# Kernel tuning notes

Hardware: AMD Instinct MI355X
Metric: run time of the kernel (lower is better)

Reference implementation:

```python
import jax, jax.numpy as jnp
import numpy as np

B, S, HID = 2, 2048, 2048
NH, NKV, HD = 16, 4, 128
ROT = 64            # head_dim * partial_rotary_factor
WINDOW = 512        # sliding_window_size
ROPE_BASE = 10000.0


def setup_inputs() -> dict:
    key = jax.random.key(0)
    ks = jax.random.split(key, 5)
    scale = 0.02
    return {
        "hidden_states": jax.random.normal(ks[0], (B, S, HID), jnp.float32),
        "Wq": jax.random.normal(ks[1], (NH * HD, HID), jnp.float32) * scale,
        "Wk": jax.random.normal(ks[2], (NKV * HD, HID), jnp.float32) * scale,
        "Wv": jax.random.normal(ks[3], (NKV * HD, HID), jnp.float32) * scale,
        "Wo": jax.random.normal(ks[4], (HID, NH * HD), jnp.float32) * scale,
    }


def _rope_cos_sin(seq_len, dtype):
    inv_freq = 1.0 / (ROPE_BASE ** (jnp.arange(0, ROT, 2, dtype=jnp.float32) / ROT))
    t = jnp.arange(seq_len, dtype=jnp.float32)
    freqs = t[:, None] * inv_freq[None, :]          # [S, ROT/2]
    emb = jnp.concatenate([freqs, freqs], axis=-1)   # [S, ROT]
    return jnp.cos(emb).astype(dtype), jnp.sin(emb).astype(dtype)


def _rotate_half(x):
    x1, x2 = x[..., : x.shape[-1] // 2], x[..., x.shape[-1] // 2:]
    return jnp.concatenate([-x2, x1], axis=-1)


def reference(hidden_states, Wq, Wk, Wv, Wo):
    b, s, _ = hidden_states.shape
    n_rep = NH // NKV

    q = (hidden_states @ Wq.T).reshape(b, s, NH, HD).transpose(0, 2, 1, 3)    # [B,NH,S,HD]
    k = (hidden_states @ Wk.T).reshape(b, s, NKV, HD).transpose(0, 2, 1, 3)   # [B,NKV,S,HD]
    v = (hidden_states @ Wv.T).reshape(b, s, NKV, HD).transpose(0, 2, 1, 3)

    # partial rotary embedding on the first ROT dims
    cos, sin = _rope_cos_sin(s, q.dtype)   # [S, ROT]
    cos = cos[None, None]                  # broadcast over batch, heads
    sin = sin[None, None]
    q_rot, q_pass = q[..., :ROT], q[..., ROT:]
    k_rot, k_pass = k[..., :ROT], k[..., ROT:]
    q_rot = q_rot * cos + _rotate_half(q_rot) * sin
    k_rot = k_rot * cos + _rotate_half(k_rot) * sin
    q = jnp.concatenate([q_rot, q_pass], axis=-1)
    k = jnp.concatenate([k_rot, k_pass], axis=-1)

    # GQA: repeat kv heads
    k = jnp.repeat(k, n_rep, axis=1)   # [B,NH,S,HD]
    v = jnp.repeat(v, n_rep, axis=1)

    scores = jnp.einsum("bhqd,bhkd->bhqk", q, k) / jnp.sqrt(jnp.asarray(HD, q.dtype))

    # sliding-window causal mask: allow j in [i-WINDOW+1, i]
    i = jnp.arange(s)[:, None]
    j = jnp.arange(s)[None, :]
    allowed = (j <= i) & (j > i - WINDOW)
    scores = jnp.where(allowed[None, None], scores, -jnp.inf)

    attn = jax.nn.softmax(scores.astype(jnp.float32), axis=-1).astype(q.dtype)
    out = jnp.einsum("bhqk,bhkd->bhqd", attn, v)          # [B,NH,S,HD]
    out = out.transpose(0, 2, 1, 3).reshape(b, s, NH * HD)
    return out @ Wo.T
```

## Files before the change

kernel.cpp:

```cpp
#include <hip/hip_runtime.h>
#include <cstdint>
#include <cstddef>

typedef __bf16 bf16;
typedef __attribute__((ext_vector_type(8))) __bf16 bf16x8;
typedef __attribute__((ext_vector_type(4))) __bf16 bf16x4;
typedef __attribute__((ext_vector_type(4))) float f32x4;
typedef __attribute__((ext_vector_type(4))) short s16x4;

#define S_LEN   2048
#define WIN     512
#define NH_Q    16
#define NH_KV   4
#define HD_     128
#define NTOK    4096

#if defined(__has_builtin)
#if __has_builtin(__builtin_amdgcn_mfma_f32_16x16x16bf16_1k)
#define HAVE_MFMA16 1
#endif
#endif
#ifndef HAVE_MFMA16
#define HAVE_MFMA16 0
#endif

#define WAIT_VM4   0x0F74
#define WAIT_VM2   0x0F72
#define WAIT_VM0   0x0F70
#define CFENCE() __asm__ __volatile__("" ::: "memory")

__device__ __forceinline__ void async_copy16(const void* g, void* l) {
  __builtin_amdgcn_global_load_lds(
      (const __attribute__((address_space(1))) void*)g,
      (__attribute__((address_space(3))) void*)l, 16, 0, 0);
}

__global__ __launch_bounds__(256)
void cvt_all(const float* __restrict__ hs, const float* __restrict__ wq,
             const float* __restrict__ wk, const float* __restrict__ wv,
             const float* __restrict__ wo, bf16* __restrict__ hsb,
             bf16* __restrict__ wqb, bf16* __restrict__ wkb,
             bf16* __restrict__ wvb, bf16* __restrict__ wob) {
  long i = ((long)blockIdx.x * 256 + threadIdx.x) * 4;
  const float* in;
  bf16* out;
  if (i < 8388608)       { in = hs + i;            out = hsb + i; }
  else if (i < 12582912) { in = wq + (i - 8388608); out = wqb + (i - 8388608); }
  else if (i < 13631488) { in = wk + (i - 12582912); out = wkb + (i - 12582912); }
  else if (i < 14680064) { in = wv + (i - 13631488); out = wvb + (i - 13631488); }
  else                   { in = wo + (i - 14680064); out = wob + (i - 14680064); }
  float4 v = *(const float4*)in;
  bf16x4 t = {(bf16)v.x, (bf16)v.y, (bf16)v.z, (bf16)v.w};
  *(bf16x4*)out = t;
}

template <typename OutT>
__global__ __launch_bounds__(256)
void gemm_bt(const bf16* __restrict__ A, const bf16* __restrict__ W,
             OutT* __restrict__ C, int M, int N, int K) {
  __shared__ __align__(16) bf16 As[2][128 * 32];
  __shared__ __align__(16) bf16 Bs[2][128 * 32];
  const int tid  = threadIdx.x;
  const int wave = tid >> 6, lane = tid & 63;
  const int quad = lane >> 4, l16 = lane & 15;
  const int wm = wave >> 1, wn = wave & 1;
  const int m0 = blockIdx.y * 128, n0 = blockIdx.x * 128;
  const int lrow = lane >> 2;
  const int lcol = (((lane & 3) + ((lane >> 3) & 3)) & 3) * 8;
  const int gfrag = ((quad - ((l16 >> 1) & 3)) & 3) * 8;

  f32x4 acc[4][4];
#pragma unroll
  for (int i = 0; i < 4; ++i)
#pragma unroll
    for (int j = 0; j < 4; ++j) acc[i][j] = (f32x4){0.f, 0.f, 0.f, 0.f};

  auto stage = [&](int buf, int k0) {
#pragma unroll
    for (int it = 0; it < 2; ++it) {
      const int c   = it * 4 + wave;
      const int row = c * 16 + lrow;
      async_copy16(A + (size_t)(m0 + row) * K + k0 + lcol, &As[buf][c * 512]);
      async_copy16(W + (size_t)(n0 + row) * K + k0 + lcol, &Bs[buf][c * 512]);
    }
  };

  stage(0, 0);
  __syncthreads();
  for (int k0 = 0; k0 < K; k0 += 32) {
    const int cur = (k0 >> 5) & 1;
    if (k0 + 32 < K) stage(cur ^ 1, k0 + 32);
    bf16x8 af[4], bfr[4];
#pragma unroll
    for (int mt = 0; mt < 4; ++mt)
      af[mt] = *(const bf16x8*)&As[cur][(wm * 64 + mt * 16 + l16) * 32 + gfrag];
#pragma unroll
    for (int nt = 0; nt < 4; ++nt)
      bfr[nt] = *(const bf16x8*)&Bs[cur][(wn * 64 + nt * 16 + l16) * 32 + gfrag];
#pragma unroll
    for (int mt = 0; mt < 4; ++mt)
#pragma unroll
      for (int nt = 0; nt < 4; ++nt)
        acc[mt][nt] = __builtin_amdgcn_mfma_f32_16x16x32_bf16(
            af[mt], bfr[nt], acc[mt][nt], 0, 0, 0);
    __syncthreads();
  }
#pragma unroll
  for (int mt = 0; mt < 4; ++mt)
#pragma unroll
    for (int nt = 0; nt < 4; ++nt)
#pragma unroll
      for (int r = 0; r < 4; ++r) {
        const int row = m0 + wm * 64 + mt * 16 + quad * 4 + r;
        const int col = n0 + wn * 64 + nt * 16 + l16;
        C[(size_t)row * N + col] = (OutT)acc[mt][nt][r];
      }
}

__global__ __launch_bounds__(512, 2)
void gemm_qkv8(const bf16* __restrict__ A, const bf16* __restrict__ Wq,
               const bf16* __restrict__ Wk, const bf16* __restrict__ Wv,
               bf16* __restrict__ Qo, bf16* __restrict__ Ko,
               bf16* __restrict__ Vt) {
  __shared__ __align__(16) char smem[131072];
  const int tid  = threadIdx.x;
  const int wave = tid >> 6, lane = tid & 63;
  const int quad = lane >> 4, l16 = lane & 15;
  const int wm = wave >> 2, wn = wave & 3;

  const int flat = blockIdx.y * 12 + blockIdx.x;
  const int swz  = (flat & 7) * 24 + (flat >> 3);
  const int m0 = (swz / 12) * 256;
  const int n0 = (swz % 12) * 256;

  const int rdb = (l16 * 64 + quad * 16) ^ ((l16 & 8) << 2);

  const int srow = lane >> 2;
  const int scol = ((lane & 3) * 8) ^ ((lane >> 5) << 4);
  const bf16* asrc = A + (size_t)(m0 + srow) * 2048 + scol;
  const bf16* aptr[2][2];
  int adst[2][2];
#pragma unroll
  for (int mh = 0; mh < 2; ++mh)
#pragma unroll
    for (int j = 0; j < 2; ++j) {
      const int rb = j * 8 + mh * 4 + (wave >> 1);
      aptr[mh][j] = asrc + (size_t)rb * 16 * 2048 + (wave & 1) * 32;
      adst[mh][j] = (rb * 2 + (wave & 1)) << 10;
    }
  const bf16* bptr[2][2];
  int bdst[2][2];
#pragma unroll
  for (int nh = 0; nh < 2; ++nh)
#pragma unroll
    for (int j = 0; j < 2; ++j) {
      const int rb = j * 8 + (wave >> 2) * 4 + nh * 2 + ((wave >> 1) & 1);
      const int nrow = n0 + rb * 16 + srow;
      const bf16* p = nrow < 2048 ? Wq + (size_t)nrow * 2048
                    : nrow < 2560 ? Wk + (size_t)(nrow - 2048) * 2048
                                  : Wv + (size_t)(nrow - 2560) * 2048;
      bptr[nh][j] = p + scol + (wave & 1) * 32;
      bdst[nh][j] = (rb * 2 + (wave & 1)) << 10;
    }

#define STAGE_A(mh, tt) do {                                        \
    char* _b = smem + ((tt) & 1) * 32768;                           \
    async_copy16(aptr[mh][0] + (tt) * 64, _b + adst[mh][0]);        \
    async_copy16(aptr[mh][1] + (tt) * 64, _b + adst[mh][1]);        \
  } while (0)
#define STAGE_B(nh, tt) do {                                        \
    char* _b = smem + 65536 + ((tt) & 1) * 32768;                   \
    async_copy16(bptr[nh][0] + (tt) * 64, _b + bdst[nh][0]);        \
    async_copy16(bptr[nh][1] + (tt) * 64, _b + bdst[nh][1]);        \
  } while (0)

  f32x4 acc[8][4];
#pragma unroll
  for (int i = 0; i < 8; ++i)
#pragma unroll
    for (int j = 0; j < 4; ++j) acc[i][j] = (f32x4){0.f, 0.f, 0.f, 0.f};

  bf16x8 afr[4][2];
  bf16x8 bfr[2][2][2];

  auto read_a = [&](const char* Ab, int mh) __attribute__((always_inline)) {
#pragma unroll
    for (int mt = 0; mt < 4; ++mt)
#pragma unroll
      for (int ks = 0; ks < 2; ++ks)
        afr[mt][ks] = *(const bf16x8*)(
            Ab + (((wm * 8 + mh * 4 + mt) * 2 + ks) << 10) + rdb);
  };
  auto read_b = [&](const char* Bb, int nh) __attribute__((always_inline)) {
#pragma unroll
    for (int nt = 0; nt < 2; ++nt)
#pragma unroll
      for (int ks = 0; ks < 2; ++ks)
        bfr[nh][nt][ks] = *(const bf16x8*)(
            Bb + (((wn * 4 + nh * 2 + nt) * 2 + ks) << 10) + rdb);
  };
  auto do_mfma = [&](int mh, int nh) __attribute__((always_inline)) {
    __builtin_amdgcn_s_setprio(1);
#pragma unroll
    for (int mt = 0; mt < 4; ++mt)
#pragma unroll
      for (int nt = 0; nt < 2; ++nt)
#pragma unroll
        for (int ks = 0; ks < 2; ++ks)
          acc[mh * 4 + mt][nh * 2 + nt] = __builtin_amdgcn_mfma_f32_16x16x32_bf16(
              afr[mt][ks], bfr[nh][nt][ks], acc[mh * 4 + mt][nh * 2 + nt],
              0, 0, 0);
    __builtin_amdgcn_s_setprio(0);
  };

  STAGE_A(0, 0); STAGE_B(0, 0); STAGE_B(1, 0); STAGE_A(1, 0);
  CFENCE();

  for (int t = 0; t < 31; ++t) {
    const char* Ab = smem + (t & 1) * 32768;
    const char* Bb = smem + 65536 + (t & 1) * 32768;
    const int nx = t + 1;
    __builtin_amdgcn_s_waitcnt(WAIT_VM4); CFENCE();
    __builtin_amdgcn_s_barrier(); CFENCE();
    read_a(Ab, 0); read_b(Bb, 0);
    STAGE_A(0, nx); CFENCE();
    do_mfma(0, 0);
    __builtin_amdgcn_s_waitcnt(WAIT_VM4); CFENCE();
    __builtin_amdgcn_s_barrier(); CFENCE();
    read_b(Bb, 1);
    STAGE_B(0, nx); CFENCE();
    do_mfma(0, 1);
    __builtin_amdgcn_s_waitcnt(WAIT_VM4); CFENCE();
    __builtin_amdgcn_s_barrier(); CFENCE();
    read_a(Ab, 1);
    STAGE_B(1, nx); CFENCE();
    do_mfma(1, 0);
    __builtin_amdgcn_s_barrier(); CFENCE();
    STAGE_A(1, nx); CFENCE();
    do_mfma(1, 1);
  }
  {
    const char* Ab = smem + 32768;
    const char* Bb = smem + 65536 + 32768;
    __builtin_amdgcn_s_waitcnt(WAIT_VM4); CFENCE();
    __builtin_amdgcn_s_barrier(); CFENCE();
    read_a(Ab, 0); read_b(Bb, 0);
    do_mfma(0, 0);
    __builtin_amdgcn_s_waitcnt(WAIT_VM2); CFENCE();
    __builtin_amdgcn_s_barrier(); CFENCE();
    read_b(Bb, 1);
    do_mfma(0, 1);
    __builtin_amdgcn_s_waitcnt(WAIT_VM0); CFENCE();
    __builtin_amdgcn_s_barrier(); CFENCE();
    read_a(Ab, 1);
    do_mfma(1, 0);
    do_mfma(1, 1);
  }
#undef STAGE_A
#undef STAGE_B

  const int cbase = n0 + wn * 64;
  if (cbase < 2560 && (cbase & 127) == 0) {
#pragma unroll
    for (int nt = 0; nt < 2; ++nt) {
      const int d = nt * 16 + l16;
      const float invf = exp2f(-(float)d * 0.41524101186091903f);
#pragma unroll
      for (int mt = 0; mt < 8; ++mt)
#pragma unroll
        for (int r = 0; r < 4; ++r) {
          const int pos = (m0 + wm * 128 + mt * 16 + quad * 4 + r) & (S_LEN - 1);
          float s, c;
          __sincosf((float)pos * invf, &s, &c);
          const float x1 = acc[mt][nt][r], x2 = acc[mt][nt + 2][r];
          acc[mt][nt][r]     = x1 * c - x2 * s;
          acc[mt][nt + 2][r] = x2 * c + x1 * s;
        }
    }
  }
#pragma unroll
  for (int mt = 0; mt < 8; ++mt) {
    const int row0 = m0 + wm * 128 + mt * 16 + quad * 4;
#pragma unroll
    for (int nt = 0; nt < 4; ++nt) {
      const int col16 = cbase + nt * 16;
      if (col16 < 2048) {
#pragma unroll
        for (int r = 0; r < 4; ++r)
          Qo[(size_t)(row0 + r) * 2048 + col16 + l16] = (bf16)acc[mt][nt][r];
      } else if (col16 < 2560) {
#pragma unroll
        for (int r = 0; r < 4; ++r)
          Ko[(size_t)(row0 + r) * 512 + col16 - 2048 + l16] = (bf16)acc[mt][nt][r];
      } else {
        const int colv = col16 + l16 - 2560;
        const int b = row0 >> 11, s0 = row0 & (S_LEN - 1);
        bf16x4 tq = {(bf16)acc[mt][nt][0], (bf16)acc[mt][nt][1],
                     (bf16)acc[mt][nt][2], (bf16)acc[mt][nt][3]};
        *(bf16x4*)(Vt + ((size_t)(b * NH_KV + (colv >> 7)) * HD_ + (colv & 127))
                        * S_LEN + s0) = tq;
      }
    }
  }
}

#define KS_STRIDE 136
#define VT_STRIDE 72

__global__ __launch_bounds__(256)
void attn_kernel(const bf16* __restrict__ Qg, const bf16* __restrict__ Kg,
                 const bf16* __restrict__ Vtg, bf16* __restrict__ Og) {
  __shared__ __align__(16) bf16 Ks[64 * KS_STRIDE];
  __shared__ __align__(16) bf16 Vt[128 * VT_STRIDE];
#if !HAVE_MFMA16
  __shared__ __align__(16) bf16 Pb[4][16 * 72];
#endif
  const int tid  = threadIdx.x;
  const int wave = tid >> 6, lane = tid & 63;
  const int quad = lane >> 4, l16 = lane & 15;
  const int qt = blockIdx.x, h = blockIdx.y, b = blockIdx.z;
  const int kv = h >> 2;
  const int q0 = qt * 64;
  const int tok0 = b * S_LEN;
  const float scale = 0.08838834764831845f;
  const int q = q0 + wave * 16 + l16;

  bf16x8 qf[4];
  {
    const bf16* qp = Qg + (size_t)(tok0 + q) * (NH_Q * HD_) + h * HD_ + quad * 8;
#pragma unroll
    for (int kb = 0; kb < 4; ++kb) qf[kb] = *(const bf16x8*)(qp + kb * 32);
  }

  f32x4 o[8];
#pragma unroll
  for (int dt = 0; dt < 8; ++dt) o[dt] = (f32x4){0.f, 0.f, 0.f, 0.f};
  float m_run = -__builtin_inff(), l_run = 0.f;

  int kt_begin = q0 - WIN;
  if (kt_begin < 0) kt_begin = 0;
  const int kt_end = q0 + 64;
  const bf16* vt_base = Vtg + (size_t)(b * NH_KV + kv) * HD_ * S_LEN;

  for (int kt = kt_begin; kt < kt_end; kt += 64) {
    __syncthreads();
#pragma unroll
    for (int it = 0; it < 4; ++it) {
      int vid = tid + it * 256;
      int key = vid >> 4, dblk = vid & 15;
      bf16x8 v = *(const bf16x8*)(Kg + (size_t)(tok0 + kt + key) * (NH_KV * HD_)
                                  + kv * HD_ + dblk * 8);
      *(bf16x8*)&Ks[key * KS_STRIDE + dblk * 8] = v;
    }
#pragma unroll
    for (int it = 0; it < 4; ++it) {
      int vid = tid + it * 256;
      int d = vid >> 3, kblk = vid & 7;
      bf16x8 v = *(const bf16x8*)(vt_base + (size_t)d * S_LEN + kt + kblk * 8);
      *(bf16x8*)&Vt[d * VT_STRIDE + kblk * 8] = v;
    }
    __syncthreads();

    f32x4 st[4];
#pragma unroll
    for (int nt = 0; nt < 4; ++nt) {
      f32x4 acc = (f32x4){0.f, 0.f, 0.f, 0.f};
#pragma unroll
      for (int kb = 0; kb < 4; ++kb) {
        bf16x8 kf = *(const bf16x8*)&Ks[(nt * 16 + l16) * KS_STRIDE + kb * 32 + quad * 8];
        acc = __builtin_amdgcn_mfma_f32_16x16x32_bf16(kf, qf[kb], acc, 0, 0, 0);
      }
      st[nt] = acc;
    }
#pragma unroll
    for (int nt = 0; nt < 4; ++nt)
#pragma unroll
      for (int r = 0; r < 4; ++r) {
        int key = kt + nt * 16 + quad * 4 + r;
        bool ok = (key <= q) && (key > q - WIN);
        st[nt][r] = ok ? st[nt][r] * scale : -__builtin_inff();
      }
    float mx = -__builtin_inff();
#pragma unroll
    for (int nt = 0; nt < 4; ++nt)
#pragma unroll
      for (int r = 0; r < 4; ++r) mx = fmaxf(mx, st[nt][r]);
    mx = fmaxf(mx, __shfl_xor(mx, 16, 64));
    mx = fmaxf(mx, __shfl_xor(mx, 32, 64));
    float mnew = fmaxf(m_run, mx);
    float msub = (mnew == -__builtin_inff()) ? 0.f : mnew;
    float alpha = __expf(m_run - msub);
    m_run = mnew;
    float p[4][4], psum = 0.f;
#pragma unroll
    for (int nt = 0; nt < 4; ++nt)
#pragma unroll
      for (int r = 0; r < 4; ++r) {
        p[nt][r] = __expf(st[nt][r] - msub);
        psum += p[nt][r];
      }
    psum += __shfl_xor(psum, 16, 64);
    psum += __shfl_xor(psum, 32, 64);
    l_run = l_run * alpha + psum;
#pragma unroll
    for (int dt = 0; dt < 8; ++dt) o[dt] *= alpha;

#if HAVE_MFMA16
    s16x4 pb[4];
#pragma unroll
    for (int nt = 0; nt < 4; ++nt)
#pragma unroll
      for (int r = 0; r < 4; ++r) {
        union { __bf16 h; short s; } u;
        u.h = (bf16)p[nt][r];
        pb[nt][r] = u.s;
      }
#pragma unroll
    for (int dt = 0; dt < 8; ++dt)
#pragma unroll
      for (int nt = 0; nt < 4; ++nt) {
        s16x4 vf = *(const s16x4*)&Vt[(dt * 16 + l16) * VT_STRIDE + nt * 16 + quad * 4];
        o[dt] = __builtin_amdgcn_mfma_f32_16x16x16bf16_1k(vf, pb[nt], o[dt], 0, 0, 0);
      }
#else
#pragma unroll
    for (int nt = 0; nt < 4; ++nt) {
      bf16x4 t;
#pragma unroll
      for (int r = 0; r < 4; ++r) t[r] = (bf16)p[nt][r];
      *(bf16x4*)&Pb[wave][l16 * 72 + nt * 16 + quad * 4] = t;
    }
    __syncthreads();
    bf16x8 pf[2];
    pf[0] = *(const bf16x8*)&Pb[wave][l16 * 72 + quad * 8];
    pf[1] = *(const bf16x8*)&Pb[wave][l16 * 72 + 32 + quad * 8];
#pragma unroll
    for (int dt = 0; dt < 8; ++dt)
#pragma unroll
      for (int kb = 0; kb < 2; ++kb) {
        bf16x8 vf = *(const bf16x8*)&Vt[(dt * 16 + l16) * VT_STRIDE + kb * 32 + quad * 8];
        o[dt] = __builtin_amdgcn_mfma_f32_16x16x32_bf16(vf, pf[kb], o[dt], 0, 0, 0);
      }
#endif
  }

  float inv = 1.f / l_run;
  __syncthreads();
#pragma unroll
  for (int dt = 0; dt < 8; ++dt) {
    bf16x4 t;
#pragma unroll
    for (int r = 0; r < 4; ++r) t[r] = (bf16)(o[dt][r] * inv);
    *(bf16x4*)&Ks[(wave * 16 + l16) * KS_STRIDE + dt * 16 + quad * 4] = t;
  }
  __syncthreads();
#pragma unroll
  for (int it = 0; it < 4; ++it) {
    int idx = tid + it * 256;
    int row = idx >> 4, chunk = idx & 15;
    bf16x8 v = *(const bf16x8*)&Ks[row * KS_STRIDE + chunk * 8];
    *(bf16x8*)(Og + (size_t)(tok0 + q0 + row) * (NH_Q * HD_) + h * HD_ + chunk * 8) = v;
  }
}

extern "C" void kernel_launch(void* const* d_in, const int* in_sizes, int n_in,
                              void* d_out, int out_size, void* d_ws, size_t ws_size,
                              hipStream_t stream) {
  const float* hs = (const float*)d_in[0];
  const float* Wq = (const float*)d_in[1];
  const float* Wk = (const float*)d_in[2];
  const float* Wv = (const float*)d_in[3];
  const float* Wo = (const float*)d_in[4];
  float* out = (float*)d_out;

  char* w = (char*)d_ws;
  bf16* hsb = (bf16*)w; w += (size_t)NTOK * 2048 * 2;
  bf16* wqb = (bf16*)w; w += (size_t)2048 * 2048 * 2;
  bf16* wkb = (bf16*)w; w += (size_t)512 * 2048 * 2;
  bf16* wvb = (bf16*)w; w += (size_t)512 * 2048 * 2;
  bf16* wob = (bf16*)w; w += (size_t)2048 * 2048 * 2;
  bf16* qb  = (bf16*)w; w += (size_t)NTOK * 2048 * 2;
  bf16* kb  = (bf16*)w; w += (size_t)NTOK * 512 * 2;
  bf16* vtb = (bf16*)w; w += (size_t)NTOK * 512 * 2;
  bf16* ab  = hsb;

  cvt_all<<<18874368 / 1024, 256, 0, stream>>>(hs, Wq, Wk, Wv, Wo,
                                               hsb, wqb, wkb, wvb, wob);

  gemm_qkv8<<<dim3(12, 16), 512, 0, stream>>>(hsb, wqb, wkb, wvb,
                                              qb, kb, vtb);

  attn_kernel<<<dim3(S_LEN / 64, NH_Q, 2), 256, 0, stream>>>(qb, kb, vtb, ab);

  gemm_bt<float><<<dim3(2048 / 128, NTOK / 128), 256, 0, stream>>>(
      ab, wob, out, NTOK, 2048, 2048);
}
```

Measured before the change: 263.9 us.

## Retile QKV GEMM to 256x192 blocks for a 256-block grid

The fused QKV projection GEMM moves from 256x256 tiles (192 blocks) to 256x192 tiles (256 blocks) so the grid fills all 256 CUs of the MI355X evenly. Warps are rearranged to a 4x2 layout, each computing 64x96, and the B staging, LDS buffer sizes, wait counts and RoPE/store epilogue are remapped to match. Smaller tiles lower arithmetic intensity per block and change the global-to-LDS copy balance between warps, which is the cost taken on for better CU occupancy.

```diff
diff --git a/kernel.cpp b/kernel.cpp
--- a/kernel.cpp
+++ b/kernel.cpp
@@ -25,6 +25,7 @@
 #endif
 
 #define WAIT_VM4   0x0F74
+#define WAIT_VM3   0x0F73
 #define WAIT_VM2   0x0F72
 #define WAIT_VM0   0x0F70
 #define CFENCE() __asm__ __volatile__("" ::: "memory")
@@ -118,186 +119,191 @@
 }
 
 __global__ __launch_bounds__(512, 2)
-void gemm_qkv8(const bf16* __restrict__ A, const bf16* __restrict__ Wq,
+void gemm_qkv9(const bf16* __restrict__ A, const bf16* __restrict__ Wq,
                const bf16* __restrict__ Wk, const bf16* __restrict__ Wv,
                bf16* __restrict__ Qo, bf16* __restrict__ Ko,
                bf16* __restrict__ Vt) {
-  __shared__ __align__(16) char smem[131072];
+  __shared__ __align__(16) char smem[114688];
   const int tid  = threadIdx.x;
   const int wave = tid >> 6, lane = tid & 63;
   const int quad = lane >> 4, l16 = lane & 15;
-  const int wm = wave >> 2, wn = wave & 3;
-
-  const int flat = blockIdx.y * 12 + blockIdx.x;
-  const int swz  = (flat & 7) * 24 + (flat >> 3);
-  const int m0 = (swz / 12) * 256;
-  const int n0 = (swz % 12) * 256;
+  const int wm = wave >> 1, wn = wave & 1;
+
+  const int flat = blockIdx.y * 16 + blockIdx.x;
+  const int swz  = (flat & 7) * 32 + (flat >> 3);
+  const int m0 = (swz >> 4) * 256;
+  const int n0 = (swz & 15) * 192;
 
   const int rdb = (l16 * 64 + quad * 16) ^ ((l16 & 8) << 2);
 
   const int srow = lane >> 2;
   const int scol = ((lane & 3) * 8) ^ ((lane >> 5) << 4);
-  const bf16* asrc = A + (size_t)(m0 + srow) * 2048 + scol;
-  const bf16* aptr[2][2];
-  int adst[2][2];
-#pragma unroll
-  for (int mh = 0; mh < 2; ++mh)
-#pragma unroll
-    for (int j = 0; j < 2; ++j) {
-      const int rb = j * 8 + mh * 4 + (wave >> 1);
-      aptr[mh][j] = asrc + (size_t)rb * 16 * 2048 + (wave & 1) * 32;
-      adst[mh][j] = (rb * 2 + (wave & 1)) << 10;
-    }
-  const bf16* bptr[2][2];
-  int bdst[2][2];
-#pragma unroll
-  for (int nh = 0; nh < 2; ++nh)
-#pragma unroll
-    for (int j = 0; j < 2; ++j) {
-      const int rb = j * 8 + (wave >> 2) * 4 + nh * 2 + ((wave >> 1) & 1);
-      const int nrow = n0 + rb * 16 + srow;
-      const bf16* p = nrow < 2048 ? Wq + (size_t)nrow * 2048
-                    : nrow < 2560 ? Wk + (size_t)(nrow - 2048) * 2048
-                                  : Wv + (size_t)(nrow - 2560) * 2048;
-      bptr[nh][j] = p + scol + (wave & 1) * 32;
-      bdst[nh][j] = (rb * 2 + (wave & 1)) << 10;
-    }
-
-#define STAGE_A(mh, tt) do {                                        \
-    char* _b = smem + ((tt) & 1) * 32768;                           \
-    async_copy16(aptr[mh][0] + (tt) * 64, _b + adst[mh][0]);        \
-    async_copy16(aptr[mh][1] + (tt) * 64, _b + adst[mh][1]);        \
-  } while (0)
-#define STAGE_B(nh, tt) do {                                        \
-    char* _b = smem + 65536 + ((tt) & 1) * 32768;                   \
-    async_copy16(bptr[nh][0] + (tt) * 64, _b + bdst[nh][0]);        \
-    async_copy16(bptr[nh][1] + (tt) * 64, _b + bdst[nh][1]);        \
-  } while (0)
-
-  f32x4 acc[8][4];
-#pragma unroll
-  for (int i = 0; i < 8; ++i)
-#pragma unroll
-    for (int j = 0; j < 4; ++j) acc[i][j] = (f32x4){0.f, 0.f, 0.f, 0.f};
-
-  bf16x8 afr[4][2];
-  bf16x8 bfr[2][2][2];
+
+  const int rbA0 = (wave >> 1) * 4 + (wave & 1);
+  const int rbA1 = rbA0 + 2;
+  const bf16* a0p = A + (size_t)(m0 + rbA0 * 16 + srow) * 2048 + scol;
+  const bf16* a1p = A + (size_t)(m0 + rbA1 * 16 + srow) * 2048 + scol;
+  const int da0 = (rbA0 * 2) << 10;
+  const int da1 = (rbA1 * 2) << 10;
+
+  const int rbB0 = wave >> 1, khB0 = wave & 1;
+  const int rbB1 = 4 + wave;
+  const int nrow0 = n0 + rbB0 * 16 + srow;
+  const int nrow1 = n0 + rbB1 * 16 + srow;
+  const bf16* b0p = (nrow0 < 2048 ? Wq + (size_t)nrow0 * 2048
+                   : nrow0 < 2560 ? Wk + (size_t)(nrow0 - 2048) * 2048
+                                  : Wv + (size_t)(nrow0 - 2560) * 2048)
+                    + scol + khB0 * 32;
+  const bf16* b1p = (nrow1 < 2048 ? Wq + (size_t)nrow1 * 2048
+                   : nrow1 < 2560 ? Wk + (size_t)(nrow1 - 2048) * 2048
+                                  : Wv + (size_t)(nrow1 - 2560) * 2048)
+                    + scol;
+  const int db0 = (rbB0 * 2 + khB0) << 10;
+  const int db1 = (rbB1 * 2) << 10;
+
+#define STAGE_A0(tt) do { char* _b = smem + ((tt) & 1) * 32768;        \
+    async_copy16(a0p + (tt) * 64,      _b + da0);                      \
+    async_copy16(a0p + (tt) * 64 + 32, _b + da0 + 1024); } while (0)
+#define STAGE_A1(tt) do { char* _b = smem + ((tt) & 1) * 32768;        \
+    async_copy16(a1p + (tt) * 64,      _b + da1);                      \
+    async_copy16(a1p + (tt) * 64 + 32, _b + da1 + 1024); } while (0)
+#define STAGE_B0(tt) do { char* _b = smem + 65536 + ((tt) & 1) * 24576; \
+    async_copy16(b0p + (tt) * 64,      _b + db0); } while (0)
+#define STAGE_B12(tt) do { char* _b = smem + 65536 + ((tt) & 1) * 24576; \
+    async_copy16(b1p + (tt) * 64,      _b + db1);                      \
+    async_copy16(b1p + (tt) * 64 + 32, _b + db1 + 1024); } while (0)
+
+  f32x4 acc[4][6];
+#pragma unroll
+  for (int i = 0; i < 4; ++i)
+#pragma unroll
+    for (int j = 0; j < 6; ++j) acc[i][j] = (f32x4){0.f, 0.f, 0.f, 0.f};
+
+  bf16x8 afr[2][2];
+  bf16x8 bfr[6][2];
 
   auto read_a = [&](const char* Ab, int mh) __attribute__((always_inline)) {
 #pragma unroll
-    for (int mt = 0; mt < 4; ++mt)
+    for (int mt2 = 0; mt2 < 2; ++mt2)
 #pragma unroll
       for (int ks = 0; ks < 2; ++ks)
-        afr[mt][ks] = *(const bf16x8*)(
-            Ab + (((wm * 8 + mh * 4 + mt) * 2 + ks) << 10) + rdb);
+        afr[mt2][ks] = *(const bf16x8*)(
+            Ab + (((wm * 4 + mh * 2 + mt2) * 2 + ks) << 10) + rdb);
   };
-  auto read_b = [&](const char* Bb, int nh) __attribute__((always_inline)) {
-#pragma unroll
-    for (int nt = 0; nt < 2; ++nt)
+  auto read_b = [&](const char* Bb, int jlo, int jhi) __attribute__((always_inline)) {
+#pragma unroll
+    for (int j = 0; j < 6; ++j) {
+      if (j < jlo || j > jhi) continue;
+      const int cc = (j >> 1) * 4 + (j & 1) * 2 + wn;
 #pragma unroll
       for (int ks = 0; ks < 2; ++ks)
-        bfr[nh][nt][ks] = *(const bf16x8*)(
-            Bb + (((wn * 4 + nh * 2 + nt) * 2 + ks) << 10) + rdb);
+        bfr[j][ks] = *(const bf16x8*)(Bb + ((cc * 2 + ks) << 10) + rdb);
+    }
   };
-  auto do_mfma = [&](int mh, int nh) __attribute__((always_inline)) {
+  auto do_mfma = [&](int mh, int jlo, int jhi) __attribute__((always_inline)) {
     __builtin_amdgcn_s_setprio(1);
 #pragma unroll
-    for (int mt = 0; mt < 4; ++mt)
-#pragma unroll
-      for (int nt = 0; nt < 2; ++nt)
+    for (int mt2 = 0; mt2 < 2; ++mt2)
+#pragma unroll
+      for (int j = 0; j < 6; ++j) {
+        if (j < jlo || j > jhi) continue;
 #pragma unroll
         for (int ks = 0; ks < 2; ++ks)
-          acc[mh * 4 + mt][nh * 2 + nt] = __builtin_amdgcn_mfma_f32_16x16x32_bf16(
-              afr[mt][ks], bfr[nh][nt][ks], acc[mh * 4 + mt][nh * 2 + nt],
-              0, 0, 0);
+          acc[mh * 2 + mt2][j] = __builtin_amdgcn_mfma_f32_16x16x32_bf16(
+              afr[mt2][ks], bfr[j][ks], acc[mh * 2 + mt2][j], 0, 0, 0);
+      }
     __builtin_amdgcn_s_setprio(0);
   };
 
-  STAGE_A(0, 0); STAGE_B(0, 0); STAGE_B(1, 0); STAGE_A(1, 0);
+  STAGE_A0(0); STAGE_B0(0); STAGE_B12(0); STAGE_A1(0);
   CFENCE();
 
   for (int t = 0; t < 31; ++t) {
     const char* Ab = smem + (t & 1) * 32768;
-    const char* Bb = smem + 65536 + (t & 1) * 32768;
+    const char* Bb = smem + 65536 + (t & 1) * 24576;
     const int nx = t + 1;
     __builtin_amdgcn_s_waitcnt(WAIT_VM4); CFENCE();
     __builtin_amdgcn_s_barrier(); CFENCE();
-    read_a(Ab, 0); read_b(Bb, 0);
-    STAGE_A(0, nx); CFENCE();
-    do_mfma(0, 0);
+    read_a(Ab, 0); read_b(Bb, 0, 1);
+    STAGE_A0(nx); CFENCE();
+    do_mfma(0, 0, 1);
     __builtin_amdgcn_s_waitcnt(WAIT_VM4); CFENCE();
     __builtin_amdgcn_s_barrier(); CFENCE();
-    read_b(Bb, 1);
-    STAGE_B(0, nx); CFENCE();
-    do_mfma(0, 1);
-    __builtin_amdgcn_s_waitcnt(WAIT_VM4); CFENCE();
+    read_b(Bb, 2, 5);
+    STAGE_B0(nx); CFENCE();
+    do_mfma(0, 2, 5);
+    __builtin_amdgcn_s_waitcnt(WAIT_VM3); CFENCE();
     __builtin_amdgcn_s_barrier(); CFENCE();
     read_a(Ab, 1);
-    STAGE_B(1, nx); CFENCE();
-    do_mfma(1, 0);
-    __builtin_amdgcn_s_barrier(); CFENCE();
-    STAGE_A(1, nx); CFENCE();
-    do_mfma(1, 1);
+    STAGE_B12(nx); CFENCE();
+    do_mfma(1, 0, 1);
+    __builtin_amdgcn_s_barrier(); CFENCE();
+    STAGE_A1(nx); CFENCE();
+    do_mfma(1, 2, 5);
   }
   {
     const char* Ab = smem + 32768;
-    const char* Bb = smem + 65536 + 32768;
+    const char* Bb = smem + 65536 + 24576;
     __builtin_amdgcn_s_waitcnt(WAIT_VM4); CFENCE();
     __builtin_amdgcn_s_barrier(); CFENCE();
-    read_a(Ab, 0); read_b(Bb, 0);
-    do_mfma(0, 0);
+    read_a(Ab, 0); read_b(Bb, 0, 1);
+    do_mfma(0, 0, 1);
     __builtin_amdgcn_s_waitcnt(WAIT_VM2); CFENCE();
     __builtin_amdgcn_s_barrier(); CFENCE();
-    read_b(Bb, 1);
-    do_mfma(0, 1);
+    read_b(Bb, 2, 5);
+    do_mfma(0, 2, 5);
     __builtin_amdgcn_s_waitcnt(WAIT_VM0); CFENCE();
     __builtin_amdgcn_s_barrier(); CFENCE();
     read_a(Ab, 1);
-    do_mfma(1, 0);
-    do_mfma(1, 1);
-  }
-#undef STAGE_A
-#undef STAGE_B
-
-  const int cbase = n0 + wn * 64;
-  if (cbase < 2560 && (cbase & 127) == 0) {
-#pragma unroll
-    for (int nt = 0; nt < 2; ++nt) {
-      const int d = nt * 16 + l16;
-      const float invf = exp2f(-(float)d * 0.41524101186091903f);
-#pragma unroll
-      for (int mt = 0; mt < 8; ++mt)
-#pragma unroll
-        for (int r = 0; r < 4; ++r) {
-          const int pos = (m0 + wm * 128 + mt * 16 + quad * 4 + r) & (S_LEN - 1);
-          float s, c;
-          __sincosf((float)pos * invf, &s, &c);
-          const float x1 = acc[mt][nt][r], x2 = acc[mt][nt + 2][r];
-          acc[mt][nt][r]     = x1 * c - x2 * s;
-          acc[mt][nt + 2][r] = x2 * c + x1 * s;
-        }
-    }
-  }
-#pragma unroll
-  for (int mt = 0; mt < 8; ++mt) {
-    const int row0 = m0 + wm * 128 + mt * 16 + quad * 4;
-#pragma unroll
-    for (int nt = 0; nt < 4; ++nt) {
-      const int col16 = cbase + nt * 16;
+    do_mfma(1, 0, 1);
+    do_mfma(1, 2, 5);
+  }
+#undef STAGE_A0
+#undef STAGE_A1
+#undef STAGE_B0
+#undef STAGE_B12
+
+  {
+    const float d = (float)(wn * 16 + l16);
+    const float invf = exp2f(-d * 0.41524101186091903f);
+#pragma unroll
+    for (int b = 0; b < 3; ++b) {
+      const int cb = n0 + b * 64;
+      if (cb < 2560 && (cb & 127) == 0) {
+#pragma unroll
+        for (int mt = 0; mt < 4; ++mt)
+#pragma unroll
+          for (int r = 0; r < 4; ++r) {
+            const int pos = (m0 + wm * 64 + mt * 16 + quad * 4 + r) & (S_LEN - 1);
+            float s, c;
+            __sincosf((float)pos * invf, &s, &c);
+            const float x1 = acc[mt][2 * b][r], x2 = acc[mt][2 * b + 1][r];
+            acc[mt][2 * b][r]     = x1 * c - x2 * s;
+            acc[mt][2 * b + 1][r] = x2 * c + x1 * s;
+          }
+      }
+    }
+  }
+#pragma unroll
+  for (int mt = 0; mt < 4; ++mt) {
+    const int row0 = m0 + wm * 64 + mt * 16 + quad * 4;
+#pragma unroll
+    for (int j = 0; j < 6; ++j) {
+      const int col16 = n0 + (j >> 1) * 64 + ((j & 1) * 2 + wn) * 16;
       if (col16 < 2048) {
 #pragma unroll
         for (int r = 0; r < 4; ++r)
-          Qo[(size_t)(row0 + r) * 2048 + col16 + l16] = (bf16)acc[mt][nt][r];
+          Qo[(size_t)(row0 + r) * 2048 + col16 + l16] = (bf16)acc[mt][j][r];
       } else if (col16 < 2560) {
 #pragma unroll
         for (int r = 0; r < 4; ++r)
-          Ko[(size_t)(row0 + r) * 512 + col16 - 2048 + l16] = (bf16)acc[mt][nt][r];
+          Ko[(size_t)(row0 + r) * 512 + col16 - 2048 + l16] = (bf16)acc[mt][j][r];
       } else {
         const int colv = col16 + l16 - 2560;
-        const int b = row0 >> 11, s0 = row0 & (S_LEN - 1);
-        bf16x4 tq = {(bf16)acc[mt][nt][0], (bf16)acc[mt][nt][1],
-                     (bf16)acc[mt][nt][2], (bf16)acc[mt][nt][3]};
-        *(bf16x4*)(Vt + ((size_t)(b * NH_KV + (colv >> 7)) * HD_ + (colv & 127))
+        const int bb = row0 >> 11, s0 = row0 & (S_LEN - 1);
+        bf16x4 tq = {(bf16)acc[mt][j][0], (bf16)acc[mt][j][1],
+                     (bf16)acc[mt][j][2], (bf16)acc[mt][j][3]};
+        *(bf16x4*)(Vt + ((size_t)(bb * NH_KV + (colv >> 7)) * HD_ + (colv & 127))
                         * S_LEN + s0) = tq;
       }
     }
@@ -487,7 +493,7 @@
   cvt_all<<<18874368 / 1024, 256, 0, stream>>>(hs, Wq, Wk, Wv, Wo,
                                                hsb, wqb, wkb, wvb, wob);
 
-  gemm_qkv8<<<dim3(12, 16), 512, 0, stream>>>(hsb, wqb, wkb, wvb,
+  gemm_qkv9<<<dim3(16, 16), 512, 0, stream>>>(hsb, wqb, wkb, wvb,
                                               qb, kb, vtb);
 
   attn_kernel<<<dim3(S_LEN / 64, NH_Q, 2), 256, 0, stream>>>(qb, kb, vtb, ab);
```

Result: faster. 256.4 us (-2.8%).
